# Optimization experiments

Measured on AMD Instinct MI355X. Metric: run time of the kernel, lower is better.

Reference implementation:

```python
import jax, jax.numpy as jnp
import numpy as np

B, N, L, C, K = 2, 8192, 8192, 128, 8
RADIUS = 0.4

def _gather(t, idx):
    # t: [B,L,D], idx: [B,N,K] -> [B,N,K,D]
    b, n, k = idx.shape
    return jnp.take_along_axis(t, idx.reshape(b, n * k)[:, :, None], axis=1).reshape(b, n, k, t.shape[-1])

def _ln(x, g, b):
    m = x.mean(-1, keepdims=True)
    v = x.var(-1, keepdims=True)
    return (x - m) * jax.lax.rsqrt(v + 1e-5) * g + b

def setup_inputs() -> dict:
    key = jax.random.key(0)
    ks = jax.random.split(key, 16)
    F = 4 * C
    def w(k, i, o):
        return jax.random.normal(k, (i, o), jnp.float32) / np.sqrt(i).astype(np.float32)
    return {
        "q_xyz": jax.random.uniform(ks[0], (B, N, 3), jnp.float32),
        "q_feat": jax.random.normal(ks[1], (B, N, C), jnp.float32),
        "kv_xyz": jax.random.uniform(ks[2], (B, L, 3), jnp.float32),
        "kv_feat": jax.random.normal(ks[3], (B, L, C), jnp.float32),
        "kv_pad": jnp.zeros((B, L), bool),
        "pos_w1": w(ks[4], 3, C), "pos_b1": jnp.zeros((C,), jnp.float32),
        "pos_w2": w(ks[5], C, C), "pos_b2": jnp.zeros((C,), jnp.float32),
        "attn_w": w(ks[6], C, C), "attn_b": jnp.zeros((C,), jnp.float32),
        "lin_w": w(ks[7], C, C),
        "lin_src_w": w(ks[8], C, C),
        "lin_dst_w": w(ks[9], C, C),
        "ln1_g": jnp.ones((C,), jnp.float32), "ln1_b": jnp.zeros((C,), jnp.float32),
        "ffn_w1": w(ks[10], C, F), "ffn_b1": jnp.zeros((F,), jnp.float32),
        "ffn_w2": w(ks[11], F, C), "ffn_b2": jnp.zeros((C,), jnp.float32),
        "ln2_g": jnp.ones((C,), jnp.float32), "ln2_b": jnp.zeros((C,), jnp.float32),
    }

def reference(q_xyz, q_feat, kv_xyz, kv_feat, kv_pad,
              pos_w1, pos_b1, pos_w2, pos_b2, attn_w, attn_b,
              lin_w, lin_src_w, lin_dst_w, ln1_g, ln1_b,
              ffn_w1, ffn_b1, ffn_w2, ffn_b2, ln2_g, ln2_b):
    # --- radius graph: up to K nearest kv points within RADIUS per query ---
    d2 = jnp.sum((q_xyz[:, :, None, :] - kv_xyz[:, None, :, :]) ** 2, -1)  # [B,N,L]
    ok = (d2 <= RADIUS ** 2) & (~kv_pad)[:, None, :]
    neg_d2, idx = jax.lax.top_k(jnp.where(ok, -d2, -jnp.inf), K)  # [B,N,K]
    ev = jnp.isfinite(neg_d2)  # edge-valid mask [B,N,K]

    # --- PointTransformerConv (vector attention, per-edge) ---
    pos_j = _gather(kv_xyz, idx)                           # [B,N,K,3]
    rel = q_xyz[:, :, None, :] - pos_j                     # pos_i - pos_j
    # pos_nn: MLP([3,C,C], plain_last=False) => ReLU after each Linear
    delta = jax.nn.relu(jax.nn.relu(rel @ pos_w1 + pos_b1) @ pos_w2 + pos_b2)  # [B,N,K,C]
    a_src = _gather(kv_feat @ lin_src_w, idx)              # [B,N,K,C]
    a_dst = q_feat @ lin_dst_w                             # [B,N,C]
    x_j = _gather(kv_feat @ lin_w, idx)                    # [B,N,K,C]
    # attn_nn: MLP([C,C], plain_last=False) => Linear + ReLU
    alpha = jax.nn.relu((a_dst[:, :, None, :] - a_src + delta) @ attn_w + attn_b)
    # segment softmax over the K neighbors (invalid edges masked out)
    scores = jnp.where(ev[..., None], alpha, -jnp.inf)
    mx = jnp.max(scores, axis=2, keepdims=True)
    mx = jnp.where(jnp.isfinite(mx), mx, 0.0)
    e = jnp.where(ev[..., None], jnp.exp(scores - mx), 0.0)
    attn = e / jnp.maximum(e.sum(2, keepdims=True), 1e-12)
    agg = jnp.sum(attn * (x_j + delta), axis=2)            # [B,N,C]

    # --- residual + LN + FFN + LN (dropout = identity at eval) ---
    out = _ln(q_feat + agg, ln1_g, ln1_b)
    h = jax.nn.gelu(out @ ffn_w1 + ffn_b1, approximate=False) @ ffn_w2 + ffn_b2
    return _ln(out + h, ln2_g, ln2_b)
```

## Files before the change

### kernel.cpp

```cpp
#include <hip/hip_runtime.h>
#include <math.h>

#define NB 2
#define NQ 8192
#define NL 8192
#define NC 128
#define NKN 8
#define NF 512
#define MQ (NB*NQ)

typedef __attribute__((ext_vector_type(8))) short bf16x8;
typedef __attribute__((ext_vector_type(4))) float f32x4;

__device__ __forceinline__ unsigned short f2bf_u(float f){
    unsigned u = __float_as_uint(f);
    return (unsigned short)((u + 0x7FFFu + ((u>>16)&1u)) >> 16);
}
__device__ __forceinline__ float bf2f(unsigned short s){
    return __uint_as_float(((unsigned)s) << 16);
}


__device__ __forceinline__ int cell_coord(float x) {
    int c = (int)(x * 16.0f);
    return min(15, max(0, c));
}

__global__ __launch_bounds__(256) void grid_count_kernel(
    const float* __restrict__ kxyz, const unsigned char* __restrict__ pad,
    int* __restrict__ cnt)
{
    int t = blockIdx.x*256 + threadIdx.x;
    if (pad[t]) return;
    int bat = t >> 13;
    float x = kxyz[t*3+0], y = kxyz[t*3+1], z = kxyz[t*3+2];
    int cell = (cell_coord(z)*16 + cell_coord(y))*16 + cell_coord(x);
    atomicAdd(&cnt[bat*4096 + cell], 1);
}

__global__ __launch_bounds__(1024) void grid_scan_kernel(
    const int* __restrict__ cnt, int* __restrict__ cs)
{
    __shared__ int wsum[17];
    int t = threadIdx.x;
    int v[8]; int s = 0;
    #pragma unroll
    for (int k = 0; k < 8; ++k) { v[k] = s; s += cnt[t*8 + k]; }
    int lane = t & 63, w = t >> 6;
    int inc = s;
    #pragma unroll
    for (int d = 1; d < 64; d <<= 1) {
        int o = __shfl_up(inc, d);
        if (lane >= d) inc += o;
    }
    if (lane == 63) wsum[w] = inc;
    __syncthreads();
    if (t == 0) {
        int a = 0;
        for (int i = 0; i < 16; ++i) { int x = wsum[i]; wsum[i] = a; a += x; }
        wsum[16] = a;
    }
    __syncthreads();
    int base = wsum[w] + (inc - s);
    #pragma unroll
    for (int k = 0; k < 8; ++k) cs[t*8 + k] = base + v[k];
    if (t == 1023) cs[8192] = wsum[16];
}

__global__ __launch_bounds__(256) void grid_scatter_kernel(
    const float* __restrict__ kxyz, const unsigned char* __restrict__ pad,
    const int* __restrict__ cs, int* __restrict__ fill, float4* __restrict__ ro)
{
    int t = blockIdx.x*256 + threadIdx.x;
    if (pad[t]) return;
    int bat = t >> 13, i = t & 8191;
    float x = kxyz[t*3+0], y = kxyz[t*3+1], z = kxyz[t*3+2];
    int cell = bat*4096 + (cell_coord(z)*16 + cell_coord(y))*16 + cell_coord(x);
    int pos = cs[cell] + atomicAdd(&fill[cell], 1);
    ro[pos] = make_float4(x, y, z, __int_as_float(i));
}

__device__ __forceinline__ void insert8(float cd, int id, float dk[8], int ik[8]) {
    if (cd < dk[7]) {
        dk[7] = cd; ik[7] = id;
        #pragma unroll
        for (int r = 6; r >= 0; --r) {
            bool sw = dk[r+1] < dk[r];
            float td = dk[r]; int ti = ik[r];
            dk[r]   = sw ? dk[r+1] : dk[r];
            ik[r]   = sw ? ik[r+1] : ik[r];
            dk[r+1] = sw ? td : dk[r+1];
            ik[r+1] = sw ? ti : ik[r+1];
        }
    }
}

template<int W>
__device__ __forceinline__ void scan_block(int l, int cx, int cy, int cz,
    float qx, float qy, float qz, const int* __restrict__ CS,
    const float4* __restrict__ RO, float dk[8], int ik[8])
{
    const int D = 2*W + 1;
    int xs = max(0, cx - W), xe = min(15, cx + W);
    int nx = xe - xs + 1;
    for (int r = l; r < D*D; r += 8) {
        int dz = r / D - W, dy = r % D - W;
        int zz = cz + dz, yy = cy + dy;
        if ((unsigned)zz > 15u || (unsigned)yy > 15u) continue;
        int c0 = (zz*16 + yy)*16 + xs;
        int s = CS[c0], e = CS[c0 + nx];
        for (int p = s; p < e; ++p) {
            float4 v = RO[p];
            float dx = qx - v.x, dyv = qy - v.y, dzv = qz - v.z;
            float cd = dx*dx + dyv*dyv + dzv*dzv;
            insert8(cd, __float_as_int(v.w), dk, ik);
        }
    }
}

__device__ __forceinline__ void merge8(float dk[8], int ik[8]) {
    #pragma unroll
    for (int m = 1; m <= 4; m <<= 1) {
        float od[8]; int oi[8];
        #pragma unroll
        for (int r = 0; r < 8; ++r) {
            od[r] = __shfl_xor(dk[r], m);
            oi[r] = __shfl_xor(ik[r], m);
        }
        float nd[8]; int ni[8];
        #pragma unroll
        for (int r = 0; r < 8; ++r) {
            bool take = od[7-r] < dk[r];
            nd[r] = take ? od[7-r] : dk[r];
            ni[r] = take ? oi[7-r] : ik[r];
        }
        #pragma unroll
        for (int st = 4; st >= 1; st >>= 1) {
            #pragma unroll
            for (int r = 0; r < 8; ++r) {
                if ((r & st) == 0 && (r | st) < 8) {
                    int b = r | st;
                    bool sw = nd[b] < nd[r];
                    float td = nd[r]; int ti = ni[r];
                    nd[r] = sw ? nd[b] : nd[r];
                    ni[r] = sw ? ni[b] : ni[r];
                    nd[b] = sw ? td : nd[b];
                    ni[b] = sw ? ti : ni[b];
                }
            }
        }
        #pragma unroll
        for (int r = 0; r < 8; ++r) { dk[r] = nd[r]; ik[r] = ni[r]; }
    }
}

__global__ __launch_bounds__(256) void prep_all_kernel(
    const float* __restrict__ posw2, const float* __restrict__ attnw,
    const float* __restrict__ lin_w, const float* __restrict__ lin_src_w,
    const float* __restrict__ lin_dst_w,
    const float* __restrict__ ffn_w1, const float* __restrict__ ffn_w2,
    unsigned short* __restrict__ imgb, int* __restrict__ zero_p)
{
    int t = blockIdx.x*256 + threadIdx.x;
    if (t < 16384) {
        int k = t >> 7, n = t & 127;
        imgb[(k >> 5)*4096 + n*32 + (k & 31)] = f2bf_u(posw2[t]);
    } else if (t < 32768) {
        int u = t - 16384;
        int k = u >> 7, n = u & 127;
        imgb[16384 + (k >> 5)*4096 + n*32 + (k & 31)] = f2bf_u(attnw[u]);
    } else if (t < 65536) {
        int u = t - 32768;
        int k = u >> 8, n = u & 255;
        float v = (n < 128) ? lin_w[k*128 + n] : lin_src_w[k*128 + (n-128)];
        imgb[32768 + ((k >> 5)*256 + n)*32 + (k & 31)] = f2bf_u(v);
    } else if (t < 81920) {
        int u = t - 65536;
        int k = u >> 7, n = u & 127;
        imgb[65536 + ((k >> 5)*128 + n)*32 + (k & 31)] = f2bf_u(lin_dst_w[u]);
    } else if (t < 147456) {
        int u = t - 81920;
        int k = u >> 9, n = u & 511;
        imgb[81920 + ((k >> 5)*512 + n)*32 + (k & 31)] = f2bf_u(ffn_w1[u]);
    } else if (t < 212992) {
        int u = t - 147456;
        int k = u >> 7, n = u & 127;
        imgb[147456 + ((k >> 5)*128 + n)*32 + (k & 31)] = f2bf_u(ffn_w2[u]);
    } else {
        zero_p[t - 212992] = 0;
    }
}

__global__ __launch_bounds__(256) void query_lin3_kernel(
    const float* __restrict__ qxyz, const int* __restrict__ cellstart,
    const float4* __restrict__ reorder, int* __restrict__ idxout,
    const float* __restrict__ kv_feat, const float* __restrict__ q_feat,
    const unsigned short* __restrict__ wvs, const unsigned short* __restrict__ wd,
    unsigned short* __restrict__ vs, float* __restrict__ adst)
{
    __shared__ unsigned short sA[64*32];
    __shared__ unsigned short sB[256*32];
    const int tid = threadIdx.x;
    const int blk = blockIdx.x;

    if (blk < MQ/32) {
        const int l    = tid & 7;
        const int qloc = tid >> 3;
        const int gq   = blk*32 + qloc;
        const int bat  = gq >> 13;
        const float qx = qxyz[gq*3+0], qy = qxyz[gq*3+1], qz = qxyz[gq*3+2];
        const int cx = cell_coord(qx), cy = cell_coord(qy), cz = cell_coord(qz);
        const int* CS = cellstart + bat*4096;
        const float R2  = (float)(0.4*0.4);
        const float R2P = __uint_as_float(__float_as_uint(R2) + 1u);

        float dk[8]; int ik[8];
        #pragma unroll
        for (int r = 0; r < 8; ++r) { dk[r] = R2P; ik[r] = -1; }

        scan_block<2>(l, cx, cy, cz, qx, qy, qz, CS, reorder, dk, ik);
        merge8(dk, ik);
        bool done = dk[7] <= 0.015625f;

        if (!done) {
            #pragma unroll
            for (int r = 0; r < 8; ++r) { dk[r] = R2P; ik[r] = -1; }
            scan_block<4>(l, cx, cy, cz, qx, qy, qz, CS, reorder, dk, ik);
            merge8(dk, ik);
            done = dk[7] <= 0.0625f;
        }
        if (!done) {
            #pragma unroll
            for (int r = 0; r < 8; ++r) { dk[r] = R2P; ik[r] = -1; }
            scan_block<16>(l, cx, cy, cz, qx, qy, qz, CS, reorder, dk, ik);
            merge8(dk, ik);
        }

        if (l == 0) {
            int o[8];
            #pragma unroll
            for (int r = 0; r < 8; ++r) o[r] = (dk[r] <= R2) ? ik[r] : -1;
            int4 a = {o[0], o[1], o[2], o[3]};
            int4 b = {o[4], o[5], o[6], o[7]};
            *(int4*)&idxout[(size_t)gq*8 + 0] = a;
            *(int4*)&idxout[(size_t)gq*8 + 4] = b;
        }
    } else if (blk < MQ/32 + MQ/64) {
        const int w = tid >> 6, lane = tid & 63, l15 = lane & 15, quad = lane >> 4;
        const int row0 = (blk - MQ/32)*64;

        f32x4 acc[16];
        #pragma unroll
        for (int t=0;t<16;t++){ acc[t][0]=0.f; acc[t][1]=0.f; acc[t][2]=0.f; acc[t][3]=0.f; }

        for (int kc = 0; kc < 4; ++kc) {
            __syncthreads();
            #pragma unroll
            for (int it = 0; it < 2; ++it) {
                int ix = it*256 + tid;
                int r = ix >> 3, kq = ix & 7;
                float4 a4 = *(const float4*)&kv_feat[(size_t)(row0+r)*NC + kc*32 + kq*4];
                ushort4 pk = { f2bf_u(a4.x), f2bf_u(a4.y), f2bf_u(a4.z), f2bf_u(a4.w) };
                *(ushort4*)&sA[r*32 + kq*4] = pk;
            }
            const int4* bsrc = (const int4*)(wvs + (size_t)kc*256*32);
            #pragma unroll
            for (int it = 0; it < 4; ++it) {
                int o = it*256 + tid;
                ((int4*)sB)[o] = bsrc[o];
            }
            __syncthreads();
            bf16x8 af = *(const bf16x8*)&sA[(w*16 + l15)*32 + quad*8];
            #pragma unroll
            for (int t = 0; t < 16; ++t) {
                bf16x8 bf = *(const bf16x8*)&sB[(16*t + l15)*32 + quad*8];
                acc[t] = __builtin_amdgcn_mfma_f32_16x16x32_bf16(af, bf, acc[t], 0, 0, 0);
            }
        }

        const int rowb = row0 + w*16 + quad*4;
        #pragma unroll
        for (int t = 0; t < 16; ++t) {
            int col = 16*t + l15;
            #pragma unroll
            for (int r = 0; r < 4; ++r)
                vs[(size_t)(rowb+r)*256 + col] = f2bf_u(acc[t][r]);
        }
    } else {
        const int w = tid >> 6, lane = tid & 63, l15 = lane & 15, quad = lane >> 4;
        const int row0 = (blk - MQ/32 - MQ/64)*64;

        f32x4 acc[8];
        #pragma unroll
        for (int t=0;t<8;t++){ acc[t][0]=0.f; acc[t][1]=0.f; acc[t][2]=0.f; acc[t][3]=0.f; }

        for (int kc = 0; kc < 4; ++kc) {
            __syncthreads();
            #pragma unroll
            for (int it = 0; it < 2; ++it) {
                int ix = it*256 + tid;
                int r = ix >> 3, kq = ix & 7;
                float4 a4 = *(const float4*)&q_feat[(size_t)(row0+r)*NC + kc*32 + kq*4];
                ushort4 pk = { f2bf_u(a4.x), f2bf_u(a4.y), f2bf_u(a4.z), f2bf_u(a4.w) };
                *(ushort4*)&sA[r*32 + kq*4] = pk;
            }
            const int4* bsrc = (const int4*)(wd + (size_t)kc*128*32);
            #pragma unroll
            for (int it = 0; it < 2; ++it) {
                int o = it*256 + tid;
                ((int4*)sB)[o] = bsrc[o];
            }
            __syncthreads();
            bf16x8 af = *(const bf16x8*)&sA[(w*16 + l15)*32 + quad*8];
            #pragma unroll
            for (int t = 0; t < 8; ++t) {
                bf16x8 bf = *(const bf16x8*)&sB[(16*t + l15)*32 + quad*8];
                acc[t] = __builtin_amdgcn_mfma_f32_16x16x32_bf16(af, bf, acc[t], 0, 0, 0);
            }
        }

        const int rowb = row0 + w*16 + quad*4;
        #pragma unroll
        for (int t = 0; t < 8; ++t) {
            int col = 16*t + l15;
            #pragma unroll
            for (int r = 0; r < 4; ++r)
                adst[(size_t)(rowb+r)*NC + col] = acc[t][r];
        }
    }
}

__device__ inline float gelu_exact(float x) {
    return 0.5f*x*(1.0f + erff(x*0.7071067811865476f));
}

__global__ __launch_bounds__(256) void ffn_fused_kernel(
    const float* __restrict__ in1,
    const unsigned short* __restrict__ wf1, const unsigned short* __restrict__ wf2,
    const float* __restrict__ b1v, const float* __restrict__ b2v,
    const float* __restrict__ g, const float* __restrict__ bb,
    float* __restrict__ out)
{
    __shared__ unsigned short sH[8*16*136];
    __shared__ float4 sS[2][16];
    __shared__ float4 sQ[2][16];
    const int tid = threadIdx.x;
    const int w = tid >> 6, lane = tid & 63, l15 = lane & 15, quad = lane >> 4;
    const int row0 = blockIdx.x*32;

    bf16x8 af0[4], af1[4];
    {
        const float* arow0 = in1 + (size_t)(row0 + l15)*NC;
        const float* arow1 = in1 + (size_t)(row0 + 16 + l15)*NC;
        #pragma unroll
        for (int kk = 0; kk < 4; ++kk) {
            float4 a0 = *(const float4*)&arow0[kk*32 + quad*8];
            float4 a1 = *(const float4*)&arow0[kk*32 + quad*8 + 4];
            bf16x8 v;
            v[0]=(short)f2bf_u(a0.x); v[1]=(short)f2bf_u(a0.y);
            v[2]=(short)f2bf_u(a0.z); v[3]=(short)f2bf_u(a0.w);
            v[4]=(short)f2bf_u(a1.x); v[5]=(short)f2bf_u(a1.y);
            v[6]=(short)f2bf_u(a1.z); v[7]=(short)f2bf_u(a1.w);
            af0[kk] = v;
            float4 b0 = *(const float4*)&arow1[kk*32 + quad*8];
            float4 b1 = *(const float4*)&arow1[kk*32 + quad*8 + 4];
            bf16x8 u;
            u[0]=(short)f2bf_u(b0.x); u[1]=(short)f2bf_u(b0.y);
            u[2]=(short)f2bf_u(b0.z); u[3]=(short)f2bf_u(b0.w);
            u[4]=(short)f2bf_u(b1.x); u[5]=(short)f2bf_u(b1.y);
            u[6]=(short)f2bf_u(b1.z); u[7]=(short)f2bf_u(b1.w);
            af1[kk] = u;
        }
    }

    f32x4 acc1a[8], acc1b[8];
    #pragma unroll
    for (int t=0;t<8;t++){
        acc1a[t][0]=0.f; acc1a[t][1]=0.f; acc1a[t][2]=0.f; acc1a[t][3]=0.f;
        acc1b[t][0]=0.f; acc1b[t][1]=0.f; acc1b[t][2]=0.f; acc1b[t][3]=0.f;
    }
    #pragma unroll
    for (int kk=0;kk<4;kk++){
        #pragma unroll
        for (int t=0;t<8;t++){
            int n = w*128 + 16*t + l15;
            bf16x8 bf = *(const bf16x8*)&wf1[((size_t)kk*512 + n)*32 + quad*8];
            acc1a[t] = __builtin_amdgcn_mfma_f32_16x16x32_bf16(af0[kk], bf, acc1a[t], 0, 0, 0);
            acc1b[t] = __builtin_amdgcn_mfma_f32_16x16x32_bf16(af1[kk], bf, acc1b[t], 0, 0, 0);
        }
    }

    {
        unsigned short* Hw0 = sH + (w)*(16*136);
        unsigned short* Hw1 = sH + (4 + w)*(16*136);
        #pragma unroll
        for (int t=0;t<8;t++){
            float bv = b1v[w*128 + 16*t + l15];
            #pragma unroll
            for (int r=0;r<4;r++){
                float x0 = gelu_exact(acc1a[t][r] + bv);
                Hw0[(quad*4+r)*136 + 16*t + l15] = f2bf_u(x0);
                float x1 = gelu_exact(acc1b[t][r] + bv);
                Hw1[(quad*4+r)*136 + 16*t + l15] = f2bf_u(x1);
            }
        }
    }
    __syncthreads();

    f32x4 acc2a[2], acc2b[2];
    #pragma unroll
    for (int tt=0;tt<2;tt++){
        acc2a[tt][0]=0.f; acc2a[tt][1]=0.f; acc2a[tt][2]=0.f; acc2a[tt][3]=0.f;
        acc2b[tt][0]=0.f; acc2b[tt][1]=0.f; acc2b[tt][2]=0.f; acc2b[tt][3]=0.f;
    }
    #pragma unroll
    for (int kkg=0;kkg<16;kkg++){
        const unsigned short* Ht0 = sH + (kkg>>2)*(16*136);
        const unsigned short* Ht1 = sH + (4 + (kkg>>2))*(16*136);
        bf16x8 a2a = *(const bf16x8*)&Ht0[l15*136 + (kkg&3)*32 + quad*8];
        bf16x8 a2b = *(const bf16x8*)&Ht1[l15*136 + (kkg&3)*32 + quad*8];
        #pragma unroll
        for (int tt=0;tt<2;tt++){
            int col = (2*w+tt)*16 + l15;
            bf16x8 bf = *(const bf16x8*)&wf2[((size_t)kkg*128 + col)*32 + quad*8];
            acc2a[tt] = __builtin_amdgcn_mfma_f32_16x16x32_bf16(a2a, bf, acc2a[tt], 0, 0, 0);
            acc2b[tt] = __builtin_amdgcn_mfma_f32_16x16x32_bf16(a2b, bf, acc2b[tt], 0, 0, 0);
        }
    }

    float xv[2][2][4];
    float Ssum[2][4], Qsum[2][4];
    #pragma unroll
    for (int tile=0; tile<2; ++tile){
        #pragma unroll
        for (int r=0;r<4;r++){ Ssum[tile][r]=0.f; Qsum[tile][r]=0.f; }
        #pragma unroll
        for (int tt=0;tt<2;tt++){
            int col = (2*w+tt)*16 + l15;
            float bv = b2v[col];
            #pragma unroll
            for (int r=0;r<4;r++){
                int row = row0 + tile*16 + quad*4 + r;
                float a = (tile==0) ? acc2a[tt][r] : acc2b[tt][r];
                float x = a + bv + in1[(size_t)row*NC + col];
                xv[tile][tt][r] = x;
                Ssum[tile][r] += x; Qsum[tile][r] += x*x;
            }
        }
        #pragma unroll
        for (int m=1;m<=8;m<<=1){
            #pragma unroll
            for (int r=0;r<4;r++){
                Ssum[tile][r] += __shfl_xor(Ssum[tile][r], m);
                Qsum[tile][r] += __shfl_xor(Qsum[tile][r], m);
            }
        }
        if (l15 == 0){
            sS[tile][w*4 + quad] = make_float4(Ssum[tile][0],Ssum[tile][1],Ssum[tile][2],Ssum[tile][3]);
            sQ[tile][w*4 + quad] = make_float4(Qsum[tile][0],Qsum[tile][1],Qsum[tile][2],Qsum[tile][3]);
        }
    }
    __syncthreads();

    #pragma unroll
    for (int tile=0; tile<2; ++tile){
        float4 St = sS[tile][quad]; float4 Qt = sQ[tile][quad];
        {
            float4 a = sS[tile][4+quad],  b = sS[tile][8+quad],  c = sS[tile][12+quad];
            St.x += a.x+b.x+c.x; St.y += a.y+b.y+c.y; St.z += a.z+b.z+c.z; St.w += a.w+b.w+c.w;
            float4 d = sQ[tile][4+quad], e = sQ[tile][8+quad],  f = sQ[tile][12+quad];
            Qt.x += d.x+e.x+f.x; Qt.y += d.y+e.y+f.y; Qt.z += d.z+e.z+f.z; Qt.w += d.w+e.w+f.w;
        }
        float mean[4], rstd[4];
        {
            float sv[4] = {St.x, St.y, St.z, St.w};
            float qv[4] = {Qt.x, Qt.y, Qt.z, Qt.w};
            #pragma unroll
            for (int r=0;r<4;r++){
                float m_ = sv[r]*(1.f/128.f);
                float v_ = qv[r]*(1.f/128.f) - m_*m_;
                mean[r] = m_;
                rstd[r] = rsqrtf(v_ + 1e-5f);
            }
        }
        #pragma unroll
        for (int tt=0;tt<2;tt++){
            int col = (2*w+tt)*16 + l15;
            float gv = g[col], bv = bb[col];
            #pragma unroll
            for (int r=0;r<4;r++){
                int row = row0 + tile*16 + quad*4 + r;
                out[(size_t)row*NC + col] = (xv[tile][tt][r]-mean[r])*rstd[r]*gv + bv;
            }
        }
    }
}

__global__ __launch_bounds__(512) void attn_mfma_kernel(
    const float* __restrict__ qxyz, const float* __restrict__ qfeat,
    const float* __restrict__ kxyz,
    const float* __restrict__ posw1, const float* __restrict__ posb1,
    const float* __restrict__ posb2, const float* __restrict__ attnb,
    const float* __restrict__ ln1g, const float* __restrict__ ln1b,
    const unsigned short* __restrict__ wimg1, const unsigned short* __restrict__ wimg2,
    const int* __restrict__ idx, const unsigned short* __restrict__ vs,
    const float* __restrict__ adst, float* __restrict__ out1)
{
    __shared__ unsigned short s_w[2*16384];
    __shared__ unsigned short s_V[8*16*136];
    __shared__ unsigned short s_T[8*16*136];
    __shared__ __align__(16) float s_w1[384];
    __shared__ __align__(16) float s_b1[128];
    __shared__ float s_b2[128], s_ab[128], s_g[128], s_bb[128];
    __shared__ int   s_j[128];

    const int tid  = threadIdx.x;
    const int w    = tid >> 6;
    const int lane = tid & 63;
    const int l15  = lane & 15;
    const int quad = lane >> 4;
    const int qbase = blockIdx.x*16 + w*2;
    const int bat  = (blockIdx.x*16) >> 13;

    if (tid < 128) {
        s_b1[tid] = posb1[tid]; s_b2[tid] = posb2[tid];
        s_ab[tid] = attnb[tid]; s_g[tid] = ln1g[tid]; s_bb[tid] = ln1b[tid];
    } else if (tid < 256) {
        int i = tid - 128;
        s_w1[i] = posw1[i]; s_w1[128+i] = posw1[128+i]; s_w1[256+i] = posw1[256+i];
    }
    if (tid < 128) s_j[tid] = idx[(size_t)blockIdx.x*128 + tid];
    #pragma unroll
    for (int r = 0; r < 4; ++r) {
        ((int4*)s_w)[r*512 + tid] = ((const int4*)wimg1)[r*512 + tid];
        ((int4*)(s_w + 16384))[r*512 + tid] = ((const int4*)wimg2)[r*512 + tid];
    }
    __syncthreads();

    #pragma unroll
    for (int i = 0; i < 4; ++i) {
        int ix = lane + i*64;
        int el = ix >> 4, c16 = ix & 15;
        int j = s_j[w*16 + el];
        int jc = j < 0 ? 0 : j;
        const int4* rp = (const int4*)(vs + ((size_t)(bat*NL + jc))*256);
        int dst = (w*16 + el)*136 + c16*8;
        *(int4*)&s_V[dst] = rp[c16];
        *(int4*)&s_T[dst] = rp[16 + c16];
    }

    bf16x8 h1f[4];
    {
        int e  = w*16 + l15;
        int qh = qbase + (l15 >> 3);
        int j  = s_j[e];
        int jc = j < 0 ? 0 : j;
        const float* kp = kxyz + ((size_t)(bat*NL + jc))*3;
        float rx = qxyz[qh*3+0]-kp[0], ry = qxyz[qh*3+1]-kp[1], rz = qxyz[qh*3+2]-kp[2];
        #pragma unroll
        for (int kk=0;kk<4;kk++){
            int c0 = kk*32 + quad*8;
            #pragma unroll
            for (int h=0; h<2; ++h){
                float4 bb4 = *(const float4*)&s_b1[c0 + h*4];
                float4 wx4 = *(const float4*)&s_w1[c0 + h*4];
                float4 wy4 = *(const float4*)&s_w1[128 + c0 + h*4];
                float4 wz4 = *(const float4*)&s_w1[256 + c0 + h*4];
                float v0 = fmaxf(bb4.x + rx*wx4.x + ry*wy4.x + rz*wz4.x, 0.f);
                float v1 = fmaxf(bb4.y + rx*wx4.y + ry*wy4.y + rz*wz4.y, 0.f);
                float v2 = fmaxf(bb4.z + rx*wx4.z + ry*wy4.z + rz*wz4.z, 0.f);
                float v3 = fmaxf(bb4.w + rx*wx4.w + ry*wy4.w + rz*wz4.w, 0.f);
                h1f[kk][h*4+0] = (short)f2bf_u(v0);
                h1f[kk][h*4+1] = (short)f2bf_u(v1);
                h1f[kk][h*4+2] = (short)f2bf_u(v2);
                h1f[kk][h*4+3] = (short)f2bf_u(v3);
            }
        }
    }

    f32x4 acc[8];
    #pragma unroll
    for (int t=0;t<8;t++){ acc[t][0]=0.f; acc[t][1]=0.f; acc[t][2]=0.f; acc[t][3]=0.f; }
    #pragma unroll
    for (int kk=0;kk<4;kk++){
        #pragma unroll
        for (int t=0;t<8;t++){
            bf16x8 wf = *(const bf16x8*)&s_w[kk*4096 + (16*t + l15)*32 + quad*8];
            acc[t] = __builtin_amdgcn_mfma_f32_16x16x32_bf16(h1f[kk], wf, acc[t], 0, 0, 0);
        }
    }

    f32x4 dreg[8];
    #pragma unroll
    for (int t=0;t<8;t++){
        float b2v = s_b2[16*t + l15];
        #pragma unroll
        for (int r=0;r<4;r++) dreg[t][r] = fmaxf(acc[t][r] + b2v, 0.f);
    }

    bool val[4];
    #pragma unroll
    for (int r=0;r<4;r++){
        int j = s_j[w*16 + quad*4 + r];
        val[r] = (j >= 0);
    }
    const int qt = qbase + (quad >> 1);
    float ad[8];
    #pragma unroll
    for (int t=0;t<8;t++) ad[t] = adst[(size_t)qt*NC + 16*t + l15];

    {
        unsigned short* st = s_T + w*16*136;
        #pragma unroll
        for (int t=0;t<8;t++){
            #pragma unroll
            for (int r=0;r<4;r++){
                int o = (quad*4 + r)*136 + 16*t + l15;
                float sv = bf2f(st[o]);
                st[o] = f2bf_u(ad[t] - sv + dreg[t][r]);
            }
        }
    }

    f32x4 acc2[8];
    #pragma unroll
    for (int t=0;t<8;t++){ acc2[t][0]=0.f; acc2[t][1]=0.f; acc2[t][2]=0.f; acc2[t][3]=0.f; }
    {
        const unsigned short* st = s_T + w*16*136;
        const unsigned short* w2 = s_w + 16384;
        #pragma unroll
        for (int kk=0;kk<4;kk++){
            bf16x8 tf = *(const bf16x8*)&st[l15*136 + kk*32 + quad*8];
            #pragma unroll
            for (int t=0;t<8;t++){
                bf16x8 wf = *(const bf16x8*)&w2[kk*4096 + (16*t + l15)*32 + quad*8];
                acc2[t] = __builtin_amdgcn_mfma_f32_16x16x32_bf16(tf, wf, acc2[t], 0, 0, 0);
            }
        }
    }

    float ex[8][4]; float dnm[8];
    #pragma unroll
    for (int t=0;t<8;t++){
        float ab = s_ab[16*t + l15];
        float s0 = val[0] ? fmaxf(acc2[t][0] + ab, 0.f) : -INFINITY;
        float s1 = val[1] ? fmaxf(acc2[t][1] + ab, 0.f) : -INFINITY;
        float s2 = val[2] ? fmaxf(acc2[t][2] + ab, 0.f) : -INFINITY;
        float s3 = val[3] ? fmaxf(acc2[t][3] + ab, 0.f) : -INFINITY;
        float mx = fmaxf(fmaxf(s0,s1), fmaxf(s2,s3));
        mx = fmaxf(mx, __shfl_xor(mx, 16));
        if (mx < -1e37f) mx = 0.f;
        ex[t][0] = __expf(s0 - mx);
        ex[t][1] = __expf(s1 - mx);
        ex[t][2] = __expf(s2 - mx);
        ex[t][3] = __expf(s3 - mx);
        float sm = ex[t][0]+ex[t][1]+ex[t][2]+ex[t][3];
        sm += __shfl_xor(sm, 16);
        dnm[t] = fmaxf(sm, 1e-12f);
    }

    float part[8];
    #pragma unroll
    for (int t=0;t<8;t++){
        float p = 0.f;
        #pragma unroll
        for (int r=0;r<4;r++){
            float vv = bf2f(s_V[(w*16 + quad*4 + r)*136 + 16*t + l15]);
            p += ex[t][r] * (vv + dreg[t][r]);
        }
        p += __shfl_xor(p, 16);
        part[t] = p / dnm[t];
    }

    float xln[8];
    float S = 0.f;
    #pragma unroll
    for (int t=0;t<8;t++){
        xln[t] = qfeat[(size_t)qt*NC + 16*t + l15] + part[t];
        S += xln[t];
    }
    #pragma unroll
    for (int m=1;m<=8;m<<=1) S += __shfl_xor(S, m);
    float mean = S * (1.f/128.f);
    float V = 0.f;
    #pragma unroll
    for (int t=0;t<8;t++){ float d = xln[t]-mean; V += d*d; }
    #pragma unroll
    for (int m=1;m<=8;m<<=1) V += __shfl_xor(V, m);
    float rstd = rsqrtf(V*(1.f/128.f) + 1e-5f);

    if ((quad & 1) == 0){
        #pragma unroll
        for (int t=0;t<8;t++){
            int c = 16*t + l15;
            out1[(size_t)qt*NC + c] = (xln[t]-mean)*rstd*s_g[c] + s_bb[c];
        }
    }
}

extern "C" void kernel_launch(void* const* d_in, const int* in_sizes, int n_in,
                              void* d_out, int out_size, void* d_ws, size_t ws_size,
                              hipStream_t stream)
{
    (void)in_sizes; (void)n_in; (void)out_size; (void)ws_size;
    const float* q_xyz   = (const float*)d_in[0];
    const float* q_feat  = (const float*)d_in[1];
    const float* kv_xyz  = (const float*)d_in[2];
    const float* kv_feat = (const float*)d_in[3];
    const unsigned char* kv_pad = (const unsigned char*)d_in[4];
    const float* pos_w1  = (const float*)d_in[5];
    const float* pos_b1  = (const float*)d_in[6];
    const float* pos_w2  = (const float*)d_in[7];
    const float* pos_b2  = (const float*)d_in[8];
    const float* attn_w  = (const float*)d_in[9];
    const float* attn_b  = (const float*)d_in[10];
    const float* lin_w   = (const float*)d_in[11];
    const float* lin_src_w = (const float*)d_in[12];
    const float* lin_dst_w = (const float*)d_in[13];
    const float* ln1_g   = (const float*)d_in[14];
    const float* ln1_b   = (const float*)d_in[15];
    const float* ffn_w1  = (const float*)d_in[16];
    const float* ffn_b1  = (const float*)d_in[17];
    const float* ffn_w2  = (const float*)d_in[18];
    const float* ffn_b2  = (const float*)d_in[19];
    const float* ln2_g   = (const float*)d_in[20];
    const float* ln2_b   = (const float*)d_in[21];

    float* ws    = (float*)d_ws;
    int*   idx   = (int*)d_ws;
    unsigned short* vs = (unsigned short*)(ws + 131072);
    float* adst  = ws + 131072 + 2*2097152;
    float* out1  = adst + 2097152;
    float* Hreg  = out1 + 2097152;

    float4* reorder  = (float4*)Hreg;
    int* cellcnt   = (int*)(reorder + 16384);
    int* cellfill  = cellcnt + 8192;
    int* cellstart = cellfill + 8192;

    unsigned short* imgb  = (unsigned short*)((char*)Hreg + (1u << 20));
    unsigned short* wimg1 = imgb;
    unsigned short* wimg2 = imgb + 16384;
    unsigned short* wvs   = imgb + 32768;
    unsigned short* wd    = imgb + 65536;
    unsigned short* wf1   = imgb + 81920;
    unsigned short* wf2   = imgb + 147456;

    prep_all_kernel<<<dim3(896), dim3(256), 0, stream>>>(
        pos_w2, attn_w, lin_w, lin_src_w, lin_dst_w, ffn_w1, ffn_w2, imgb, cellcnt);

    grid_count_kernel<<<dim3(64), dim3(256), 0, stream>>>(kv_xyz, kv_pad, cellcnt);
    grid_scan_kernel<<<dim3(1), dim3(1024), 0, stream>>>(cellcnt, cellstart);
    grid_scatter_kernel<<<dim3(64), dim3(256), 0, stream>>>(kv_xyz, kv_pad, cellstart, cellfill, reorder);

    query_lin3_kernel<<<dim3(MQ/32 + MQ/64 + MQ/64), dim3(256), 0, stream>>>(
        q_xyz, cellstart, reorder, idx,
        kv_feat, q_feat, wvs, wd, vs, adst);

    attn_mfma_kernel<<<dim3(MQ/16), dim3(512), 0, stream>>>(
        q_xyz, q_feat, kv_xyz,
        pos_w1, pos_b1, pos_b2, attn_b, ln1_g, ln1_b,
        wimg1, wimg2, idx, vs, adst, out1);

    ffn_fused_kernel<<<dim3(MQ/32), dim3(256), 0, stream>>>(
        out1, wf1, wf2, ffn_b1, ffn_b2, ln2_g, ln2_b, (float*)d_out);
}
```

Measured before the change: 212.2 us.

## Fuse FFN and second LayerNorm into attention kernel epilogue

The separate FFN kernel is removed and its work is appended to the attention kernel. Each 16-query block keeps the LN1 output in shared memory (as bf16 for the MFMA operand and fp32 for the residual), then runs both FFN matmuls, GELU and LN2 in place. This drops the out1 round trip through global memory and one kernel launch. In exchange, shared memory use rises, each block now reloads the FFN weights for only 16 rows instead of 32, and the attention kernel gets longer with extra barriers, which may lower occupancy.

```diff
diff --git a/kernel.cpp b/kernel.cpp
--- a/kernel.cpp
+++ b/kernel.cpp
@@ -18,6 +18,10 @@
 }
 __device__ __forceinline__ float bf2f(unsigned short s){
     return __uint_as_float(((unsigned)s) << 16);
+}
+
+__device__ inline float gelu_exact(float x) {
+    return 0.5f*x*(1.0f + erff(x*0.7071067811865476f));
 }
 
 
@@ -330,173 +334,7 @@
     }
 }
 
-__device__ inline float gelu_exact(float x) {
-    return 0.5f*x*(1.0f + erff(x*0.7071067811865476f));
-}
-
-__global__ __launch_bounds__(256) void ffn_fused_kernel(
-    const float* __restrict__ in1,
-    const unsigned short* __restrict__ wf1, const unsigned short* __restrict__ wf2,
-    const float* __restrict__ b1v, const float* __restrict__ b2v,
-    const float* __restrict__ g, const float* __restrict__ bb,
-    float* __restrict__ out)
-{
-    __shared__ unsigned short sH[8*16*136];
-    __shared__ float4 sS[2][16];
-    __shared__ float4 sQ[2][16];
-    const int tid = threadIdx.x;
-    const int w = tid >> 6, lane = tid & 63, l15 = lane & 15, quad = lane >> 4;
-    const int row0 = blockIdx.x*32;
-
-    bf16x8 af0[4], af1[4];
-    {
-        const float* arow0 = in1 + (size_t)(row0 + l15)*NC;
-        const float* arow1 = in1 + (size_t)(row0 + 16 + l15)*NC;
-        #pragma unroll
-        for (int kk = 0; kk < 4; ++kk) {
-            float4 a0 = *(const float4*)&arow0[kk*32 + quad*8];
-            float4 a1 = *(const float4*)&arow0[kk*32 + quad*8 + 4];
-            bf16x8 v;
-            v[0]=(short)f2bf_u(a0.x); v[1]=(short)f2bf_u(a0.y);
-            v[2]=(short)f2bf_u(a0.z); v[3]=(short)f2bf_u(a0.w);
-            v[4]=(short)f2bf_u(a1.x); v[5]=(short)f2bf_u(a1.y);
-            v[6]=(short)f2bf_u(a1.z); v[7]=(short)f2bf_u(a1.w);
-            af0[kk] = v;
-            float4 b0 = *(const float4*)&arow1[kk*32 + quad*8];
-            float4 b1 = *(const float4*)&arow1[kk*32 + quad*8 + 4];
-            bf16x8 u;
-            u[0]=(short)f2bf_u(b0.x); u[1]=(short)f2bf_u(b0.y);
-            u[2]=(short)f2bf_u(b0.z); u[3]=(short)f2bf_u(b0.w);
-            u[4]=(short)f2bf_u(b1.x); u[5]=(short)f2bf_u(b1.y);
-            u[6]=(short)f2bf_u(b1.z); u[7]=(short)f2bf_u(b1.w);
-            af1[kk] = u;
-        }
-    }
-
-    f32x4 acc1a[8], acc1b[8];
-    #pragma unroll
-    for (int t=0;t<8;t++){
-        acc1a[t][0]=0.f; acc1a[t][1]=0.f; acc1a[t][2]=0.f; acc1a[t][3]=0.f;
-        acc1b[t][0]=0.f; acc1b[t][1]=0.f; acc1b[t][2]=0.f; acc1b[t][3]=0.f;
-    }
-    #pragma unroll
-    for (int kk=0;kk<4;kk++){
-        #pragma unroll
-        for (int t=0;t<8;t++){
-            int n = w*128 + 16*t + l15;
-            bf16x8 bf = *(const bf16x8*)&wf1[((size_t)kk*512 + n)*32 + quad*8];
-            acc1a[t] = __builtin_amdgcn_mfma_f32_16x16x32_bf16(af0[kk], bf, acc1a[t], 0, 0, 0);
-            acc1b[t] = __builtin_amdgcn_mfma_f32_16x16x32_bf16(af1[kk], bf, acc1b[t], 0, 0, 0);
-        }
-    }
-
-    {
-        unsigned short* Hw0 = sH + (w)*(16*136);
-        unsigned short* Hw1 = sH + (4 + w)*(16*136);
-        #pragma unroll
-        for (int t=0;t<8;t++){
-            float bv = b1v[w*128 + 16*t + l15];
-            #pragma unroll
-            for (int r=0;r<4;r++){
-                float x0 = gelu_exact(acc1a[t][r] + bv);
-                Hw0[(quad*4+r)*136 + 16*t + l15] = f2bf_u(x0);
-                float x1 = gelu_exact(acc1b[t][r] + bv);
-                Hw1[(quad*4+r)*136 + 16*t + l15] = f2bf_u(x1);
-            }
-        }
-    }
-    __syncthreads();
-
-    f32x4 acc2a[2], acc2b[2];
-    #pragma unroll
-    for (int tt=0;tt<2;tt++){
-        acc2a[tt][0]=0.f; acc2a[tt][1]=0.f; acc2a[tt][2]=0.f; acc2a[tt][3]=0.f;
-        acc2b[tt][0]=0.f; acc2b[tt][1]=0.f; acc2b[tt][2]=0.f; acc2b[tt][3]=0.f;
-    }
-    #pragma unroll
-    for (int kkg=0;kkg<16;kkg++){
-        const unsigned short* Ht0 = sH + (kkg>>2)*(16*136);
-        const unsigned short* Ht1 = sH + (4 + (kkg>>2))*(16*136);
-        bf16x8 a2a = *(const bf16x8*)&Ht0[l15*136 + (kkg&3)*32 + quad*8];
-        bf16x8 a2b = *(const bf16x8*)&Ht1[l15*136 + (kkg&3)*32 + quad*8];
-        #pragma unroll
-        for (int tt=0;tt<2;tt++){
-            int col = (2*w+tt)*16 + l15;
-            bf16x8 bf = *(const bf16x8*)&wf2[((size_t)kkg*128 + col)*32 + quad*8];
-            acc2a[tt] = __builtin_amdgcn_mfma_f32_16x16x32_bf16(a2a, bf, acc2a[tt], 0, 0, 0);
-            acc2b[tt] = __builtin_amdgcn_mfma_f32_16x16x32_bf16(a2b, bf, acc2b[tt], 0, 0, 0);
-        }
-    }
-
-    float xv[2][2][4];
-    float Ssum[2][4], Qsum[2][4];
-    #pragma unroll
-    for (int tile=0; tile<2; ++tile){
-        #pragma unroll
-        for (int r=0;r<4;r++){ Ssum[tile][r]=0.f; Qsum[tile][r]=0.f; }
-        #pragma unroll
-        for (int tt=0;tt<2;tt++){
-            int col = (2*w+tt)*16 + l15;
-            float bv = b2v[col];
-            #pragma unroll
-            for (int r=0;r<4;r++){
-                int row = row0 + tile*16 + quad*4 + r;
-                float a = (tile==0) ? acc2a[tt][r] : acc2b[tt][r];
-                float x = a + bv + in1[(size_t)row*NC + col];
-                xv[tile][tt][r] = x;
-                Ssum[tile][r] += x; Qsum[tile][r] += x*x;
-            }
-        }
-        #pragma unroll
-        for (int m=1;m<=8;m<<=1){
-            #pragma unroll
-            for (int r=0;r<4;r++){
-                Ssum[tile][r] += __shfl_xor(Ssum[tile][r], m);
-                Qsum[tile][r] += __shfl_xor(Qsum[tile][r], m);
-            }
-        }
-        if (l15 == 0){
-            sS[tile][w*4 + quad] = make_float4(Ssum[tile][0],Ssum[tile][1],Ssum[tile][2],Ssum[tile][3]);
-            sQ[tile][w*4 + quad] = make_float4(Qsum[tile][0],Qsum[tile][1],Qsum[tile][2],Qsum[tile][3]);
-        }
-    }
-    __syncthreads();
-
-    #pragma unroll
-    for (int tile=0; tile<2; ++tile){
-        float4 St = sS[tile][quad]; float4 Qt = sQ[tile][quad];
-        {
-            float4 a = sS[tile][4+quad],  b = sS[tile][8+quad],  c = sS[tile][12+quad];
-            St.x += a.x+b.x+c.x; St.y += a.y+b.y+c.y; St.z += a.z+b.z+c.z; St.w += a.w+b.w+c.w;
-            float4 d = sQ[tile][4+quad], e = sQ[tile][8+quad],  f = sQ[tile][12+quad];
-            Qt.x += d.x+e.x+f.x; Qt.y += d.y+e.y+f.y; Qt.z += d.z+e.z+f.z; Qt.w += d.w+e.w+f.w;
-        }
-        float mean[4], rstd[4];
-        {
-            float sv[4] = {St.x, St.y, St.z, St.w};
-            float qv[4] = {Qt.x, Qt.y, Qt.z, Qt.w};
-            #pragma unroll
-            for (int r=0;r<4;r++){
-                float m_ = sv[r]*(1.f/128.f);
-                float v_ = qv[r]*(1.f/128.f) - m_*m_;
-                mean[r] = m_;
-                rstd[r] = rsqrtf(v_ + 1e-5f);
-            }
-        }
-        #pragma unroll
-        for (int tt=0;tt<2;tt++){
-            int col = (2*w+tt)*16 + l15;
-            float gv = g[col], bv = bb[col];
-            #pragma unroll
-            for (int r=0;r<4;r++){
-                int row = row0 + tile*16 + quad*4 + r;
-                out[(size_t)row*NC + col] = (xv[tile][tt][r]-mean[r])*rstd[r]*gv + bv;
-            }
-        }
-    }
-}
-
-__global__ __launch_bounds__(512) void attn_mfma_kernel(
+__global__ __launch_bounds__(512) void attn_ffn_kernel(
     const float* __restrict__ qxyz, const float* __restrict__ qfeat,
     const float* __restrict__ kxyz,
     const float* __restrict__ posw1, const float* __restrict__ posb1,
@@ -504,11 +342,18 @@
     const float* __restrict__ ln1g, const float* __restrict__ ln1b,
     const unsigned short* __restrict__ wimg1, const unsigned short* __restrict__ wimg2,
     const int* __restrict__ idx, const unsigned short* __restrict__ vs,
-    const float* __restrict__ adst, float* __restrict__ out1)
+    const float* __restrict__ adst,
+    const unsigned short* __restrict__ wf1, const unsigned short* __restrict__ wf2,
+    const float* __restrict__ fb1, const float* __restrict__ fb2,
+    const float* __restrict__ g2, const float* __restrict__ bb2,
+    float* __restrict__ dout)
 {
     __shared__ unsigned short s_w[2*16384];
     __shared__ unsigned short s_V[8*16*136];
     __shared__ unsigned short s_T[8*16*136];
+    __shared__ unsigned short s_X[16*136];
+    __shared__ float          s_Xf[16*132];
+    __shared__ float4 sS2[32], sQ2[32];
     __shared__ __align__(16) float s_w1[384];
     __shared__ __align__(16) float s_b1[128];
     __shared__ float s_b2[128], s_ab[128], s_g[128], s_bb[128];
@@ -690,11 +535,102 @@
     float rstd = rsqrtf(V*(1.f/128.f) + 1e-5f);
 
     if ((quad & 1) == 0){
+        int lrow = w*2 + (quad >> 1);
         #pragma unroll
         for (int t=0;t<8;t++){
             int c = 16*t + l15;
-            out1[(size_t)qt*NC + c] = (xln[t]-mean)*rstd*s_g[c] + s_bb[c];
-        }
+            float o = (xln[t]-mean)*rstd*s_g[c] + s_bb[c];
+            s_X[lrow*136 + c] = f2bf_u(o);
+            s_Xf[lrow*132 + c] = o;
+        }
+    }
+    __syncthreads();
+
+    bf16x8 axf[4];
+    #pragma unroll
+    for (int kk=0;kk<4;kk++)
+        axf[kk] = *(const bf16x8*)&s_X[l15*136 + kk*32 + quad*8];
+
+    f32x4 f1[4];
+    #pragma unroll
+    for (int t=0;t<4;t++){ f1[t][0]=0.f; f1[t][1]=0.f; f1[t][2]=0.f; f1[t][3]=0.f; }
+    #pragma unroll
+    for (int kk=0;kk<4;kk++){
+        #pragma unroll
+        for (int t=0;t<4;t++){
+            int n = w*64 + 16*t + l15;
+            bf16x8 bf = *(const bf16x8*)&wf1[((size_t)kk*512 + n)*32 + quad*8];
+            f1[t] = __builtin_amdgcn_mfma_f32_16x16x32_bf16(axf[kk], bf, f1[t], 0, 0, 0);
+        }
+    }
+
+    unsigned short* H = s_V;
+    #pragma unroll
+    for (int t=0;t<4;t++){
+        int hc = w*64 + 16*t + l15;
+        float bv = fb1[hc];
+        #pragma unroll
+        for (int r=0;r<4;r++){
+            float x = gelu_exact(f1[t][r] + bv);
+            H[(quad*4+r)*520 + hc] = f2bf_u(x);
+        }
+    }
+    __syncthreads();
+
+    f32x4 f2;
+    f2[0]=0.f; f2[1]=0.f; f2[2]=0.f; f2[3]=0.f;
+    const int ocol = w*16 + l15;
+    #pragma unroll
+    for (int kkg=0;kkg<16;kkg++){
+        bf16x8 a2 = *(const bf16x8*)&H[l15*520 + kkg*32 + quad*8];
+        bf16x8 bf = *(const bf16x8*)&wf2[((size_t)kkg*128 + ocol)*32 + quad*8];
+        f2 = __builtin_amdgcn_mfma_f32_16x16x32_bf16(a2, bf, f2, 0, 0, 0);
+    }
+
+    float xr[4];
+    float Sp0=0.f,Sp1=0.f,Sp2=0.f,Sp3=0.f;
+    float Qp0=0.f,Qp1=0.f,Qp2=0.f,Qp3=0.f;
+    {
+        float bv2 = fb2[ocol];
+        #pragma unroll
+        for (int r=0;r<4;r++){
+            int row = quad*4 + r;
+            float x = f2[r] + bv2 + s_Xf[row*132 + ocol];
+            xr[r] = x;
+            if (r==0){ Sp0+=x; Qp0+=x*x; } else if (r==1){ Sp1+=x; Qp1+=x*x; }
+            else if (r==2){ Sp2+=x; Qp2+=x*x; } else { Sp3+=x; Qp3+=x*x; }
+        }
+    }
+    #pragma unroll
+    for (int m=1;m<=8;m<<=1){
+        Sp0 += __shfl_xor(Sp0,m); Sp1 += __shfl_xor(Sp1,m);
+        Sp2 += __shfl_xor(Sp2,m); Sp3 += __shfl_xor(Sp3,m);
+        Qp0 += __shfl_xor(Qp0,m); Qp1 += __shfl_xor(Qp1,m);
+        Qp2 += __shfl_xor(Qp2,m); Qp3 += __shfl_xor(Qp3,m);
+    }
+    if (l15 == 0){
+        sS2[w*4 + quad] = make_float4(Sp0,Sp1,Sp2,Sp3);
+        sQ2[w*4 + quad] = make_float4(Qp0,Qp1,Qp2,Qp3);
+    }
+    __syncthreads();
+
+    float4 St = sS2[quad]; float4 Qt = sQ2[quad];
+    #pragma unroll
+    for (int v=1; v<8; ++v){
+        float4 a = sS2[v*4+quad], b = sQ2[v*4+quad];
+        St.x += a.x; St.y += a.y; St.z += a.z; St.w += a.w;
+        Qt.x += b.x; Qt.y += b.y; Qt.z += b.z; Qt.w += b.w;
+    }
+    float sv4[4] = {St.x, St.y, St.z, St.w};
+    float qv4[4] = {Qt.x, Qt.y, Qt.z, Qt.w};
+    float gvv = g2[ocol], bvv = bb2[ocol];
+    #pragma unroll
+    for (int r=0;r<4;r++){
+        float m_ = sv4[r]*(1.f/128.f);
+        float v_ = qv4[r]*(1.f/128.f) - m_*m_;
+        float rs = rsqrtf(v_ + 1e-5f);
+        int row = blockIdx.x*16 + quad*4 + r;
+        dout[(size_t)row*NC + ocol] = (xr[r]-m_)*rs*gvv + bvv;
     }
 }
 
@@ -757,11 +693,10 @@
         q_xyz, cellstart, reorder, idx,
         kv_feat, q_feat, wvs, wd, vs, adst);
 
-    attn_mfma_kernel<<<dim3(MQ/16), dim3(512), 0, stream>>>(
+    attn_ffn_kernel<<<dim3(MQ/16), dim3(512), 0, stream>>>(
         q_xyz, q_feat, kv_xyz,
         pos_w1, pos_b1, pos_b2, attn_b, ln1_g, ln1_b,
-        wimg1, wimg2, idx, vs, adst, out1);
-
-    ffn_fused_kernel<<<dim3(MQ/32), dim3(256), 0, stream>>>(
-        out1, wf1, wf2, ffn_b1, ffn_b2, ln2_g, ln2_b, (float*)d_out);
-}
+        wimg1, wimg2, idx, vs, adst,
+        wf1, wf2, ffn_b1, ffn_b2, ln2_g, ln2_b,
+        (float*)d_out);
+}
```

After: 214.3 us. About the same (+1.0%).
